# Optimization experiments

Measured on AMD Instinct MI355X. Metric: run time of the kernel, lower is better.

## Reference

```python
import jax, jax.numpy as jnp
import numpy as np

F = 26          # categorical fields
VOCAB = 10000   # per-field vocab
ED = 64         # embed_dim
NUM = 13        # numerical_num
B = 4096        # batch
E = 8           # expert_num
T = 2           # task_num
D = (F + 1) * ED            # embed_output_dim = 1728
BOT = [512, 256]
TOW = [128, 64]


def setup_inputs() -> dict:
    key = jax.random.key(0)
    ks = jax.random.split(key, 20)
    s = 0.02
    inp = {}
    inp['categorical_x'] = jax.random.randint(ks[0], (B, F), 0, VOCAB, dtype=jnp.int64 if jax.config.read('jax_enable_x64') else jnp.int32)
    inp['numerical_x'] = jax.random.normal(ks[1], (B, NUM), dtype=jnp.float32)
    # shared embedding table with per-field offsets (pytorch-fm EmbeddingLayer)
    inp['offsets'] = jnp.arange(F, dtype=jnp.int32) * VOCAB
    inp['W_emb'] = jax.random.normal(ks[2], (F * VOCAB, ED), dtype=jnp.float32) * s
    # numerical linear
    inp['Wn'] = jax.random.normal(ks[3], (NUM, ED), dtype=jnp.float32) * s
    inp['bn'] = jnp.zeros((ED,), dtype=jnp.float32)
    # experts (stacked): D -> 512 -> 256, ReLU after each (BN/dropout identity at eval)
    inp['We1'] = jax.random.normal(ks[4], (E, D, BOT[0]), dtype=jnp.float32) * s
    inp['be1'] = jnp.zeros((E, BOT[0]), dtype=jnp.float32)
    inp['We2'] = jax.random.normal(ks[5], (E, BOT[0], BOT[1]), dtype=jnp.float32) * s
    inp['be2'] = jnp.zeros((E, BOT[1]), dtype=jnp.float32)
    # gates: D -> E with softmax
    inp['Wg'] = jax.random.normal(ks[6], (T, D, E), dtype=jnp.float32) * s
    inp['bg'] = jnp.zeros((T, E), dtype=jnp.float32)
    # towers: 256 -> 128 -> 64 -> 1
    inp['Wt1'] = jax.random.normal(ks[7], (T, BOT[1], TOW[0]), dtype=jnp.float32) * s
    inp['bt1'] = jnp.zeros((T, TOW[0]), dtype=jnp.float32)
    inp['Wt2'] = jax.random.normal(ks[8], (T, TOW[0], TOW[1]), dtype=jnp.float32) * s
    inp['bt2'] = jnp.zeros((T, TOW[1]), dtype=jnp.float32)
    inp['Wt3'] = jax.random.normal(ks[9], (T, TOW[1], 1), dtype=jnp.float32) * s
    inp['bt3'] = jnp.zeros((T, 1), dtype=jnp.float32)
    return inp


def reference(categorical_x, numerical_x, offsets, W_emb, Wn, bn,
              We1, be1, We2, be2, Wg, bg,
              Wt1, bt1, Wt2, bt2, Wt3, bt3):
    b = categorical_x.shape[0]
    cat_emb = W_emb[categorical_x + offsets[None, :]]          # [B, F, ED]
    num_emb = numerical_x @ Wn + bn                            # [B, ED]
    emb = jnp.concatenate([cat_emb, num_emb[:, None, :]], axis=1).reshape(b, -1)  # [B, D]
    # all experts on the shared embedding (duplicate() gives identical copies per task)
    h = jax.nn.relu(jnp.einsum('bd,edh->ebh', emb, We1) + be1[:, None, :])        # [E, B, 512]
    fea = jax.nn.relu(jnp.einsum('ebh,eho->ebo', h, We2) + be2[:, None, :])       # [E, B, 256]
    # per-task softmax gating and weighted expert mixing
    gate = jax.nn.softmax(jnp.einsum('bd,tde->tbe', emb, Wg) + bg[:, None, :], axis=-1)  # [T, B, E]
    task_fea = jnp.einsum('tbe,ebo->tbo', gate, fea)                              # [T, B, 256]
    # towers
    h1 = jax.nn.relu(jnp.einsum('tbo,toh->tbh', task_fea, Wt1) + bt1[:, None, :])
    h2 = jax.nn.relu(jnp.einsum('tbh,thk->tbk', h1, Wt2) + bt2[:, None, :])
    logits = jnp.einsum('tbk,tko->tbo', h2, Wt3) + bt3[:, None, :]                # [T, B, 1]
    return jax.nn.sigmoid(logits[..., 0])                                         # [T, B]
```

## Files before the change

### kernel.cpp

```cpp
#include <hip/hip_runtime.h>
#include <hip/hip_bf16.h>

#define B_SZ 4096
#define F_CAT 26
#define NUM_N 13
#define ED 64
#define D_DIM 1728
#define E_EXP 8
#define T_TASK 2
#define BOT0 512
#define BOT1 256
#define TOW0 128
#define TOW1 64

typedef __bf16 bf16x8 __attribute__((ext_vector_type(8)));
typedef float f32x4 __attribute__((ext_vector_type(4)));
typedef float f32x16 __attribute__((ext_vector_type(16)));
typedef long lx2 __attribute__((ext_vector_type(2)));
typedef int i32x4 __attribute__((ext_vector_type(4)));
typedef int i32x8 __attribute__((ext_vector_type(8)));

#define SCL 0x7F7F7F7F

__device__ __forceinline__ void gload_lds16(const void* g, void* l) {
  __builtin_amdgcn_global_load_lds(
      (const __attribute__((address_space(1))) void*)g,
      (__attribute__((address_space(3))) void*)l, 16, 0, 0);
}

#define BAR() do { asm volatile("" ::: "memory"); __builtin_amdgcn_s_barrier(); asm volatile("" ::: "memory"); } while (0)
#define VM6() asm volatile("s_waitcnt vmcnt(6)" ::: "memory")
#define VM4() asm volatile("s_waitcnt vmcnt(4)" ::: "memory")

__device__ __forceinline__ int permk(int k6) {
  return (k6 & 7) + (((k6 >> 3) & 3) << 4) + (((k6 >> 5) & 1) << 3);
}

__device__ __forceinline__ size_t mxpos(int row, int kabs, int K) {
  int kt = kabs >> 6, kk = kabs & 63;
  int reg = row & ~63, ro = row & 63;
  int sub = ro >> 5, rr = ro & 31, r = rr & 15;
  int u = ((kk >> 5) << 1) | ((rr >> 4) & 1);
  int p = (kk >> 4) & 1;
  int g = (sub << 1) | p;
  return (size_t)(reg + g * 16 + r) * K + kt * 64 + u * 16 + (kk & 15);
}

__device__ __forceinline__ unsigned char f2e4m3(float x) {
  unsigned su = (__float_as_uint(x) >> 24) & 0x80u;
  float ax = fabsf(x);
  if (!(ax < 448.f)) return (unsigned char)(su | 0x7E);
  if (ax == 0.f) return (unsigned char)su;
  int e;
  float m = frexpf(ax, &e);
  int E = e - 1;
  if (E < -6) {
    int mi = (int)rintf(ldexpf(ax, 9));
    if (mi >= 8) return (unsigned char)(su | 0x08);
    return (unsigned char)(su | mi);
  }
  int mi = (int)rintf(ldexpf(m, 4));
  if (mi == 16) { mi = 8; E += 1; if (E > 8) return (unsigned char)(su | 0x7E); }
  return (unsigned char)(su | ((E + 7) << 3) | (mi - 8));
}

__device__ __forceinline__ void trans_tile_bf16(
    const float* __restrict__ inp, __hip_bfloat16* __restrict__ outp,
    int R, int C, int cx, int ry, float (*tile)[33])
{
  int c0 = cx * 32, r0 = ry * 32;
  int tx = threadIdx.x & 31, ty = threadIdx.x >> 5;
#pragma unroll
  for (int i = 0; i < 32; i += 8)
    tile[ty + i][tx] = inp[(size_t)(r0 + ty + i) * C + c0 + tx];
  __syncthreads();
#pragma unroll
  for (int i = 0; i < 32; i += 8)
    outp[(size_t)(c0 + ty + i) * R + r0 + tx] = __float2bfloat16(tile[tx][ty + i]);
}

__device__ __forceinline__ void trans_tile_fp8mx(
    const float* __restrict__ inp, unsigned char* __restrict__ outp,
    int R, int C, int cx, int ry, float (*tile)[33])
{
  int c0 = cx * 32, r0 = ry * 32;
  int tx = threadIdx.x & 31, ty = threadIdx.x >> 5;
#pragma unroll
  for (int i = 0; i < 32; i += 8)
    tile[ty + i][tx] = inp[(size_t)(r0 + ty + i) * C + c0 + tx];
  __syncthreads();
  int ki = r0 + tx;
#pragma unroll
  for (int i = 0; i < 32; i += 8)
    outp[mxpos(c0 + ty + i, ki, R)] = f2e4m3(tile[tx][ty + i] * 16.f);
}

__global__ __launch_bounds__(256) void prep_weights(
    const float* __restrict__ We1, const float* __restrict__ We2,
    const float* __restrict__ Wg,
    unsigned char* __restrict__ We1T8, __hip_bfloat16* __restrict__ We2T,
    unsigned char* __restrict__ WgT8)
{
  __shared__ float tile[32][33];
  int id = blockIdx.x;
  if (id < 6912) {
    int z = id / 864, r = id - z * 864;
    int cx = r & 15, ry = r >> 4;
    trans_tile_fp8mx(We1 + (size_t)z * D_DIM * BOT0, We1T8 + (size_t)z * D_DIM * BOT0,
                     D_DIM, BOT0, cx, ry, tile);
  } else if (id < 7936) {
    int r2 = id - 6912;
    int z = r2 >> 7, r = r2 & 127;
    int cx = r & 7, ry = r >> 3;
    trans_tile_bf16(We2 + (size_t)z * BOT0 * BOT1, We2T + (size_t)z * BOT0 * BOT1,
                    BOT0, BOT1, cx, ry, tile);
  } else {
    int i = (id - 7936) * 256 + threadIdx.x;
    int n = i / D_DIM, d = i - n * D_DIM;
    int t = n >> 3, e2 = n & 7;
    int pd = (d & ~63) + permk(d & 63);
    WgT8[(size_t)n * D_DIM + pd] =
        f2e4m3(Wg[((size_t)t * D_DIM + d) * E_EXP + e2] * 16.f);
  }
}

__global__ __launch_bounds__(256) void embed_convert(
    const int* __restrict__ cat, const float* __restrict__ numx,
    const int* __restrict__ offsets, const float* __restrict__ W_emb,
    const float* __restrict__ Wn, const float* __restrict__ bnum,
    unsigned char* __restrict__ emb8)
{
  int W = blockIdx.x * 256 + threadIdx.x;
  int prow = W / 108, ucol = W - prow * 108;
  int f = ucol >> 2, u = ucol & 3;
  int reg = prow & ~63, po = prow & 63;
  int g = po >> 4, r = po & 15;
  int sub = g >> 1, p = g & 1;
  int h = u >> 1, rbit = u & 1;
  int b = reg + sub * 32 + rbit * 16 + r;
  int kk = h * 32 + p * 16;
  float vals[16];
  if (f < F_CAT) {
    int row = cat[(size_t)b * F_CAT + f] + offsets[f];
    const float4* src = reinterpret_cast<const float4*>(&W_emb[(size_t)row * ED + kk]);
#pragma unroll
    for (int q = 0; q < 4; ++q) {
      float4 v = src[q];
      vals[q * 4 + 0] = v.x; vals[q * 4 + 1] = v.y;
      vals[q * 4 + 2] = v.z; vals[q * 4 + 3] = v.w;
    }
  } else {
#pragma unroll
    for (int j = 0; j < 16; ++j) vals[j] = bnum[kk + j];
    for (int n = 0; n < NUM_N; ++n) {
      float x = numx[(size_t)b * NUM_N + n];
      const float* wr = &Wn[n * ED + kk];
#pragma unroll
      for (int j = 0; j < 16; ++j) vals[j] = fmaf(x, wr[j], vals[j]);
    }
  }
  union { unsigned char c[16]; uint4 q; } o;
#pragma unroll
  for (int j = 0; j < 16; ++j) o.c[j] = f2e4m3(vals[j] * 16.f);
  *reinterpret_cast<uint4*>(&emb8[(size_t)prow * D_DIM + f * 64 + u * 16]) = o.q;
}

__global__ __launch_bounds__(256) void gate_mfma(
    const unsigned char* __restrict__ emb8, const unsigned char* __restrict__ WgT8,
    const float* __restrict__ bg, float* __restrict__ gate)
{
  int wid = threadIdx.x >> 6, lane = threadIdx.x & 63;
  int l15 = lane & 15, lh = lane >> 4;
  int r0 = (blockIdx.x * 4 + wid) * 16;
  f32x4 acc = {};
  int b = r0 + l15;
  int reg = b & ~63, ro = b & 63;
  int sub = ro >> 5, rr = ro & 31;
  int rbit = (rr >> 4) & 1, rq = rr & 15;
  int pgh = lh >> 1;
  int prow = reg + (((sub << 1) | pgh) << 4) + rq;
  const unsigned char* arow = emb8 + (size_t)prow * D_DIM + rbit * 16 + (lh & 1) * 8;
  const unsigned char* brow = WgT8 + (size_t)l15 * D_DIM + lh * 16;
#pragma unroll 3
  for (int k = 0; k < D_DIM; k += 64) {
    long a0 = *reinterpret_cast<const long*>(arow + k);
    long a1 = *reinterpret_cast<const long*>(arow + k + 32);
    lx2 bv = *reinterpret_cast<const lx2*>(brow + k);
    acc = __builtin_amdgcn_mfma_f32_16x16x32_fp8_fp8(a0, bv[0], acc, 0, 0, 0);
    acc = __builtin_amdgcn_mfma_f32_16x16x32_fp8_fp8(a1, bv[1], acc, 0, 0, 0);
  }
  int t = l15 >> 3, e = l15 & 7;
  float bv = bg[t * E_EXP + e];
#pragma unroll
  for (int r = 0; r < 4; ++r) {
    float lg = acc[r] * (1.f / 256.f) + bv;
    float m = lg;
    m = fmaxf(m, __shfl_xor(m, 1));
    m = fmaxf(m, __shfl_xor(m, 2));
    m = fmaxf(m, __shfl_xor(m, 4));
    float ex = expf(lg - m);
    float s = ex;
    s += __shfl_xor(s, 1);
    s += __shfl_xor(s, 2);
    s += __shfl_xor(s, 4);
    int row = r0 + lh * 4 + r;
    gate[((size_t)t * B_SZ + row) * E_EXP + e] = ex / s;
  }
}

__device__ __forceinline__ void mfma16(const bf16x8* a, const bf16x8* b, f32x4 (*accRows)[4]) {
#pragma unroll
  for (int i = 0; i < 4; ++i)
#pragma unroll
    for (int j = 0; j < 4; ++j)
      accRows[i][j] = __builtin_amdgcn_mfma_f32_16x16x32_bf16(a[i], b[j], accRows[i][j], 0, 0, 0);
}

__device__ __forceinline__ i32x8 ld32(const char* base, int off) {
  i32x4 a = *reinterpret_cast<const i32x4*>(base + off);
  i32x4 b = *reinterpret_cast<const i32x4*>(base + off + 1024);
  i32x8 r;
  r[0] = a[0]; r[1] = a[1]; r[2] = a[2]; r[3] = a[3];
  r[4] = b[0]; r[5] = b[1]; r[6] = b[2]; r[7] = b[3];
  return r;
}

__global__ __launch_bounds__(512, 2) void gemm_mx(
    const unsigned char* __restrict__ A8, size_t strideAe,
    const unsigned char* __restrict__ BT8,
    const float* __restrict__ bias,
    __hip_bfloat16* __restrict__ C,
    int M, int N, int K)
{
  extern __shared__ char smem[];
  int e = blockIdx.z;
  const unsigned char* Ap = A8 + strideAe * (size_t)e;
  const unsigned char* Bp = BT8 + (size_t)e * N * K;
  const float* bp = bias + (size_t)e * N;
  __hip_bfloat16* Cp = C + (size_t)e * M * N;
  int bm0 = blockIdx.x * 256, bn0 = blockIdx.y * 256;

  int tid = threadIdx.x;
  int wid = tid >> 6, lane = tid & 63;
  int l15 = lane & 15, lh = lane >> 4;
  int l31 = lane & 31, hl = lane >> 5;
  int wrow = (wid >> 2) * 128, wcol = (wid & 3) * 64;

  int slotc = (lh ^ (((l15 >> 3) & 1) << 1)) << 4;
  const char* rdA = smem + (wrow + l15) * 64 + slotc;
  const char* rdB = smem + 49152 + (wcol + l15) * 64 + slotc;
  char* stA = smem + (wid << 10);
  char* stB = smem + 49152 + (wid << 10);

  int srow = tid >> 2;
  int ssw = (tid & 3) ^ (((srow >> 3) & 1) << 1);
  const unsigned char* gA0 = Ap + (size_t)(bm0 + srow) * K + ssw * 16;
  const unsigned char* gA1 = Ap + (size_t)(bm0 + 128 + srow) * K + ssw * 16;
  const unsigned char* gB0 = Bp + (size_t)(bn0 + srow) * K + ssw * 16;
  const unsigned char* gB1 = Bp + (size_t)(bn0 + 128 + srow) * K + ssw * 16;

  auto STAGE = [&](int koff, int buf) {
    gload_lds16(gA0 + koff, stA + buf * 16384);
    gload_lds16(gA1 + koff, stA + buf * 16384 + 8192);
    gload_lds16(gB0 + koff, stB + buf * 16384);
    gload_lds16(gB1 + koff, stB + buf * 16384 + 8192);
  };

  f32x16 acc[4][2] = {};
  int NT = K >> 6;

  STAGE(0, 0);
  STAGE(64, 1);
  VM4();
  BAR();

  int bufc = 0, koff = 128;
  for (int T = 0; T < NT; ++T) {
    const char* As = rdA + bufc * 16384;
    const char* Bs = rdB + bufc * 16384;
    int sb = bufc >= 1 ? bufc - 1 : 2;
    i32x8 va0, va1, vb0, vb1;

    va0 = ld32(As, 0);
    va1 = ld32(As, 2048);
    vb0 = ld32(Bs, 0);
    vb1 = ld32(Bs, 2048);
    STAGE(koff, sb);
    BAR();
    __builtin_amdgcn_s_setprio(1);
    acc[0][0] = __builtin_amdgcn_mfma_scale_f32_32x32x64_f8f6f4(va0, vb0, acc[0][0], 0, 0, 0, SCL, 0, SCL);
    acc[0][1] = __builtin_amdgcn_mfma_scale_f32_32x32x64_f8f6f4(va0, vb1, acc[0][1], 0, 0, 0, SCL, 0, SCL);
    acc[1][0] = __builtin_amdgcn_mfma_scale_f32_32x32x64_f8f6f4(va1, vb0, acc[1][0], 0, 0, 0, SCL, 0, SCL);
    acc[1][1] = __builtin_amdgcn_mfma_scale_f32_32x32x64_f8f6f4(va1, vb1, acc[1][1], 0, 0, 0, SCL, 0, SCL);
    __builtin_amdgcn_s_setprio(0);
    BAR();

    va0 = ld32(As, 4096);
    va1 = ld32(As, 4096 + 2048);
    BAR();
    __builtin_amdgcn_s_setprio(1);
    acc[2][0] = __builtin_amdgcn_mfma_scale_f32_32x32x64_f8f6f4(va0, vb0, acc[2][0], 0, 0, 0, SCL, 0, SCL);
    acc[2][1] = __builtin_amdgcn_mfma_scale_f32_32x32x64_f8f6f4(va0, vb1, acc[2][1], 0, 0, 0, SCL, 0, SCL);
    acc[3][0] = __builtin_amdgcn_mfma_scale_f32_32x32x64_f8f6f4(va1, vb0, acc[3][0], 0, 0, 0, SCL, 0, SCL);
    acc[3][1] = __builtin_amdgcn_mfma_scale_f32_32x32x64_f8f6f4(va1, vb1, acc[3][1], 0, 0, 0, SCL, 0, SCL);
    __builtin_amdgcn_s_setprio(0);
    VM4();
    BAR();

    koff += 64;
    bufc = bufc == 2 ? 0 : bufc + 1;
  }

  asm volatile("s_waitcnt vmcnt(0)" ::: "memory");
  BAR();
  __hip_bfloat16* cs = (__hip_bfloat16*)smem;
#pragma unroll
  for (int mi = 0; mi < 4; ++mi) {
#pragma unroll
    for (int nj = 0; nj < 2; ++nj) {
      int colT = wcol + nj * 32 + l31;
      float bv = bp[bn0 + colT];
      f32x16 a = acc[mi][nj];
#pragma unroll
      for (int rg = 0; rg < 16; ++rg) {
        int rowT = wrow + mi * 32 + (rg & 3) + ((rg >> 2) << 3) + (hl << 2);
        float v = a[rg] * (1.f / 256.f) + bv;
        cs[(size_t)rowT * 256 + colT] = __float2bfloat16(fmaxf(v, 0.f));
      }
    }
  }
  BAR();
  {
    int rr = tid >> 5, c8 = (tid & 31) * 8;
#pragma unroll
    for (int p = 0; p < 16; ++p) {
      int row = p * 16 + rr;
      *reinterpret_cast<uint4*>(&Cp[(size_t)(bm0 + row) * N + bn0 + c8]) =
          *reinterpret_cast<const uint4*>(&cs[(size_t)row * 256 + c8]);
    }
  }
}

__global__ __launch_bounds__(512, 2) void gemm4p(
    const __hip_bfloat16* __restrict__ A, size_t strideAe,
    const __hip_bfloat16* __restrict__ BT,
    const float* __restrict__ bias,
    __hip_bfloat16* __restrict__ C,
    int M, int N, int K)
{
  extern __shared__ char smem[];
  int e = blockIdx.z;
  const __hip_bfloat16* Ap = A + strideAe * (size_t)e;
  const __hip_bfloat16* Bp = BT + (size_t)e * N * K;
  const float* bp = bias + (size_t)e * N;
  __hip_bfloat16* Cp = C + (size_t)e * M * N;
  int bm0 = blockIdx.x * 128, bn0 = blockIdx.y * 256;

  int tid = threadIdx.x;
  int wid = tid >> 6, lane = tid & 63;
  int l15 = lane & 15, lh = lane >> 4;
  int wrow = (wid >> 2) * 64, wcol = (wid & 3) * 64;

  int slotc = (lh ^ (((l15 >> 3) & 1) << 1)) << 4;
  const char* rdA = smem + (wrow + l15) * 64 + slotc;
  const char* rdB = smem + 32768 + (wcol + l15) * 64 + slotc;
  char* stA = smem + (wid << 10);
  char* stB = smem + 32768 + (wid << 10);

  const __hip_bfloat16* gA;
  const __hip_bfloat16* gB[2];
  {
    int X = (wid << 10) + (lane << 4);
    int row = X >> 6;
    int ss = ((X >> 4) & 3) ^ (((row >> 3) & 1) << 1);
    gA = Ap + (size_t)(bm0 + row) * K + ss * 8;
#pragma unroll
    for (int j = 0; j < 2; ++j) {
      int X2 = X + (j << 13);
      int row2 = X2 >> 6;
      int ss2 = ((X2 >> 4) & 3) ^ (((row2 >> 3) & 1) << 1);
      gB[j] = Bp + (size_t)(bn0 + row2) * K + ss2 * 8;
    }
  }

  f32x4 acc[4][4] = {};
  int NT = K >> 6;

  gload_lds16(gA, stA);
#pragma unroll
  for (int j = 0; j < 2; ++j) gload_lds16(gB[j], stB + (j << 13));
  gload_lds16(gA + 32, stA + 8192);
#pragma unroll
  for (int j = 0; j < 2; ++j) gload_lds16(gB[j] + 32, stB + 16384 + (j << 13));
  gload_lds16(gA + 64, stA + 16384);
#pragma unroll
  for (int j = 0; j < 2; ++j) gload_lds16(gB[j] + 64, stB + 32768 + (j << 13));
  VM6();
  BAR();

  for (int T = 0; T < NT; ++T) {
    int pA = (T & 1) << 14, qA = pA ^ 16384;
    int pB = (T & 1) << 15, qB = pB ^ 32768;
    const char* As = rdA + pA;
    const char* Bs = rdB + pB;
    bf16x8 a[4], b[4];

#pragma unroll
    for (int i = 0; i < 4; ++i) a[i] = *(const bf16x8*)(As + i * 1024);
#pragma unroll
    for (int j = 0; j < 4; ++j) b[j] = *(const bf16x8*)(Bs + j * 1024);
    gload_lds16(gA + 96, stA + qA + 8192);
#pragma unroll
    for (int j = 0; j < 2; ++j) gload_lds16(gB[j] + 96, stB + qB + 16384 + (j << 13));
    BAR();
    __builtin_amdgcn_s_setprio(1); mfma16(a, b, acc); __builtin_amdgcn_s_setprio(0);
    VM6();
    BAR();

#pragma unroll
    for (int i = 0; i < 4; ++i) a[i] = *(const bf16x8*)(As + 8192 + i * 1024);
#pragma unroll
    for (int j = 0; j < 4; ++j) b[j] = *(const bf16x8*)(Bs + 16384 + j * 1024);
    gload_lds16(gA + 128, stA + pA);
#pragma unroll
    for (int j = 0; j < 2; ++j) gload_lds16(gB[j] + 128, stB + pB + (j << 13));
    BAR();
    __builtin_amdgcn_s_setprio(1); mfma16(a, b, acc); __builtin_amdgcn_s_setprio(0);
    VM6();
    BAR();

    gA += 64;
#pragma unroll
    for (int j = 0; j < 2; ++j) gB[j] += 64;
  }

  asm volatile("s_waitcnt vmcnt(0)" ::: "memory");
  BAR();
  __hip_bfloat16* cs = (__hip_bfloat16*)smem;
#pragma unroll
  for (int nj = 0; nj < 4; ++nj) {
    int col = wcol + nj * 16 + l15;
    float bv = bp[bn0 + col];
#pragma unroll
    for (int mi = 0; mi < 4; ++mi) {
      int rb = wrow + mi * 16 + lh * 4;
#pragma unroll
      for (int r = 0; r < 4; ++r) {
        float v = acc[mi][nj][r] + bv;
        cs[(size_t)(rb + r) * 256 + col] = __float2bfloat16(fmaxf(v, 0.f));
      }
    }
  }
  BAR();
  {
    int rr = tid >> 5, c8 = (tid & 31) * 8;
#pragma unroll
    for (int p = 0; p < 8; ++p) {
      int row = p * 16 + rr;
      *reinterpret_cast<uint4*>(&Cp[(size_t)(bm0 + row) * N + bn0 + c8]) =
          *reinterpret_cast<const uint4*>(&cs[(size_t)row * 256 + c8]);
    }
  }
}

#define TB 16
__global__ __launch_bounds__(256) void combine_tower(
    const float* __restrict__ gate, const __hip_bfloat16* __restrict__ fea,
    const float* __restrict__ Wt1, const float* __restrict__ bt1,
    const float* __restrict__ Wt2, const float* __restrict__ bt2,
    const float* __restrict__ Wt3, const float* __restrict__ bt3,
    float* __restrict__ out)
{
  int t = blockIdx.y;
  int b0 = blockIdx.x * TB;
  int tid = threadIdx.x;
  __shared__ float gs[TB][E_EXP];
  __shared__ float tf[TB][BOT1];
  __shared__ float h1[TB][TOW0];
  __shared__ float h2[TB][TOW1];
  if (tid < TB * E_EXP) {
    int bl = tid >> 3, e = tid & 7;
    gs[bl][e] = gate[((size_t)t * B_SZ + b0 + bl) * E_EXP + e];
  }
  __syncthreads();
  for (int i = tid; i < TB * BOT1; i += 256) {
    int bl = i >> 8, o = i & 255;
    float s = 0.f;
#pragma unroll
    for (int e = 0; e < E_EXP; ++e)
      s = fmaf(gs[bl][e], __bfloat162float(fea[((size_t)e * B_SZ + b0 + bl) * BOT1 + o]), s);
    tf[bl][o] = s;
  }
  __syncthreads();
  {
    int h = tid & 127, half = tid >> 7;
    float a[8] = {0, 0, 0, 0, 0, 0, 0, 0};
    for (int d = 0; d < BOT1; ++d) {
      float w = Wt1[((size_t)t * BOT1 + d) * TOW0 + h];
#pragma unroll
      for (int q = 0; q < 8; ++q) a[q] = fmaf(w, tf[half * 8 + q][d], a[q]);
    }
    float bv = bt1[t * TOW0 + h];
#pragma unroll
    for (int q = 0; q < 8; ++q) h1[half * 8 + q][h] = fmaxf(a[q] + bv, 0.f);
  }
  __syncthreads();
  {
    int h = tid & 63, qt = tid >> 6;
    float a[4] = {0, 0, 0, 0};
    for (int d = 0; d < TOW0; ++d) {
      float w = Wt2[((size_t)t * TOW0 + d) * TOW1 + h];
#pragma unroll
      for (int q = 0; q < 4; ++q) a[q] = fmaf(w, h1[qt * 4 + q][d], a[q]);
    }
    float bv = bt2[t * TOW1 + h];
#pragma unroll
    for (int q = 0; q < 4; ++q) h2[qt * 4 + q][h] = fmaxf(a[q] + bv, 0.f);
  }
  __syncthreads();
  {
    int l16 = tid & 15, bl = tid >> 4;
    float p = 0.f;
#pragma unroll
    for (int d = l16; d < TOW1; d += 16) p = fmaf(h2[bl][d], Wt3[t * TOW1 + d], p);
#pragma unroll
    for (int o = 8; o; o >>= 1) p += __shfl_down(p, o, 16);
    if (l16 == 0) {
      float lg = p + bt3[t];
      out[(size_t)t * B_SZ + b0 + bl] = 1.f / (1.f + expf(-lg));
    }
  }
}

extern "C" void kernel_launch(void* const* d_in, const int* in_sizes, int n_in,
                              void* d_out, int out_size, void* d_ws, size_t ws_size,
                              hipStream_t stream) {
  const int* cat = (const int*)d_in[0];
  const float* numx = (const float*)d_in[1];
  const int* offsets = (const int*)d_in[2];
  const float* W_emb = (const float*)d_in[3];
  const float* Wn = (const float*)d_in[4];
  const float* bnv = (const float*)d_in[5];
  const float* We1 = (const float*)d_in[6];
  const float* be1 = (const float*)d_in[7];
  const float* We2 = (const float*)d_in[8];
  const float* be2 = (const float*)d_in[9];
  const float* Wg = (const float*)d_in[10];
  const float* bg = (const float*)d_in[11];
  const float* Wt1 = (const float*)d_in[12];
  const float* bt1 = (const float*)d_in[13];
  const float* Wt2 = (const float*)d_in[14];
  const float* bt2 = (const float*)d_in[15];
  const float* Wt3 = (const float*)d_in[16];
  const float* bt3 = (const float*)d_in[17];
  float* out = (float*)d_out;

  char* ws = (char*)d_ws;
  size_t off = 0;
  auto alloc = [&](size_t bytes) {
    char* p = ws + off;
    off += (bytes + 255) & ~(size_t)255;
    return p;
  };
  unsigned char*  emb8  = (unsigned char*)alloc((size_t)B_SZ * D_DIM);
  unsigned char*  We1T8 = (unsigned char*)alloc((size_t)E_EXP * BOT0 * D_DIM);
  __hip_bfloat16* We2T  = (__hip_bfloat16*)alloc((size_t)E_EXP * BOT1 * BOT0 * 2);
  __hip_bfloat16* H     = (__hip_bfloat16*)alloc((size_t)E_EXP * B_SZ * BOT0 * 2);
  __hip_bfloat16* fea   = (__hip_bfloat16*)alloc((size_t)E_EXP * B_SZ * BOT1 * 2);
  float* gate = (float*)alloc((size_t)T_TASK * B_SZ * E_EXP * 4);
  unsigned char*  WgT8  = (unsigned char*)alloc((size_t)T_TASK * E_EXP * D_DIM);
  (void)alloc(4096);

  hipFuncSetAttribute((const void*)gemm_mx,
                      hipFuncAttributeMaxDynamicSharedMemorySize, 131072);
  hipFuncSetAttribute((const void*)gemm4p,
                      hipFuncAttributeMaxDynamicSharedMemorySize, 98304);

  prep_weights<<<dim3(8044), 256, 0, stream>>>(We1, We2, Wg, We1T8, We2T, WgT8);

  embed_convert<<<dim3(B_SZ * 108 / 256), 256, 0, stream>>>(
      cat, numx, offsets, W_emb, Wn, bnv, emb8);

  gate_mfma<<<dim3(B_SZ / 64), 256, 0, stream>>>(emb8, WgT8, bg, gate);

  gemm_mx<<<dim3(B_SZ / 256, BOT0 / 256, E_EXP), 512, 131072, stream>>>(
      emb8, (size_t)0, We1T8, be1, H, B_SZ, BOT0, D_DIM);

  gemm4p<<<dim3(B_SZ / 128, BOT1 / 256, E_EXP), 512, 98304, stream>>>(
      H, (size_t)B_SZ * BOT0, We2T, be2, fea, B_SZ, BOT1, BOT0);

  combine_tower<<<dim3(B_SZ / TB, T_TASK), 256, 0, stream>>>(
      gate, fea, Wt1, bt1, Wt2, bt2, Wt3, bt3, out);
}
```

Before: 117.7 us.

## Quantize expert hidden layer and second GEMM to MX fp8

The first expert GEMM now writes its ReLU output as fp8 e4m3, pre-swizzled into the MX layout the next GEMM reads. The second expert GEMM moves from a bf16 16x16x32 MFMA kernel to a new 128-row fp8 scaled-MFMA kernel, and the We2 weights are prepared as fp8. This halves the traffic for the large H intermediate and the second GEMM's operands, and uses the higher-rate fp8 matrix instructions. In exchange, the hidden activations are quantized more coarsely, and the first GEMM's epilogue does a per-element scattered fp8 conversion.

```diff
diff --git a/kernel.cpp b/kernel.cpp
--- a/kernel.cpp
+++ b/kernel.cpp
@@ -29,8 +29,8 @@
 }
 
 #define BAR() do { asm volatile("" ::: "memory"); __builtin_amdgcn_s_barrier(); asm volatile("" ::: "memory"); } while (0)
-#define VM6() asm volatile("s_waitcnt vmcnt(6)" ::: "memory")
 #define VM4() asm volatile("s_waitcnt vmcnt(4)" ::: "memory")
+#define VM3() asm volatile("s_waitcnt vmcnt(3)" ::: "memory")
 
 __device__ __forceinline__ int permk(int k6) {
   return (k6 & 7) + (((k6 >> 3) & 3) << 4) + (((k6 >> 5) & 1) << 3);
@@ -64,21 +64,6 @@
   return (unsigned char)(su | ((E + 7) << 3) | (mi - 8));
 }
 
-__device__ __forceinline__ void trans_tile_bf16(
-    const float* __restrict__ inp, __hip_bfloat16* __restrict__ outp,
-    int R, int C, int cx, int ry, float (*tile)[33])
-{
-  int c0 = cx * 32, r0 = ry * 32;
-  int tx = threadIdx.x & 31, ty = threadIdx.x >> 5;
-#pragma unroll
-  for (int i = 0; i < 32; i += 8)
-    tile[ty + i][tx] = inp[(size_t)(r0 + ty + i) * C + c0 + tx];
-  __syncthreads();
-#pragma unroll
-  for (int i = 0; i < 32; i += 8)
-    outp[(size_t)(c0 + ty + i) * R + r0 + tx] = __float2bfloat16(tile[tx][ty + i]);
-}
-
 __device__ __forceinline__ void trans_tile_fp8mx(
     const float* __restrict__ inp, unsigned char* __restrict__ outp,
     int R, int C, int cx, int ry, float (*tile)[33])
@@ -98,7 +83,7 @@
 __global__ __launch_bounds__(256) void prep_weights(
     const float* __restrict__ We1, const float* __restrict__ We2,
     const float* __restrict__ Wg,
-    unsigned char* __restrict__ We1T8, __hip_bfloat16* __restrict__ We2T,
+    unsigned char* __restrict__ We1T8, unsigned char* __restrict__ We2T8,
     unsigned char* __restrict__ WgT8)
 {
   __shared__ float tile[32][33];
@@ -112,8 +97,8 @@
     int r2 = id - 6912;
     int z = r2 >> 7, r = r2 & 127;
     int cx = r & 7, ry = r >> 3;
-    trans_tile_bf16(We2 + (size_t)z * BOT0 * BOT1, We2T + (size_t)z * BOT0 * BOT1,
-                    BOT0, BOT1, cx, ry, tile);
+    trans_tile_fp8mx(We2 + (size_t)z * BOT0 * BOT1, We2T8 + (size_t)z * BOT0 * BOT1,
+                     BOT0, BOT1, cx, ry, tile);
   } else {
     int i = (id - 7936) * 256 + threadIdx.x;
     int n = i / D_DIM, d = i - n * D_DIM;
@@ -208,14 +193,6 @@
   }
 }
 
-__device__ __forceinline__ void mfma16(const bf16x8* a, const bf16x8* b, f32x4 (*accRows)[4]) {
-#pragma unroll
-  for (int i = 0; i < 4; ++i)
-#pragma unroll
-    for (int j = 0; j < 4; ++j)
-      accRows[i][j] = __builtin_amdgcn_mfma_f32_16x16x32_bf16(a[i], b[j], accRows[i][j], 0, 0, 0);
-}
-
 __device__ __forceinline__ i32x8 ld32(const char* base, int off) {
   i32x4 a = *reinterpret_cast<const i32x4*>(base + off);
   i32x4 b = *reinterpret_cast<const i32x4*>(base + off + 1024);
@@ -225,7 +202,135 @@
   return r;
 }
 
+#define MXMFMA(va, vb, c) \
+  __builtin_amdgcn_mfma_scale_f32_32x32x64_f8f6f4(va, vb, c, 0, 0, 0, SCL, 0, SCL)
+
 __global__ __launch_bounds__(512, 2) void gemm_mx(
+    const unsigned char* __restrict__ A8, size_t strideAe,
+    const unsigned char* __restrict__ BT8,
+    const float* __restrict__ bias,
+    unsigned char* __restrict__ C8,
+    int M, int N, int K)
+{
+  extern __shared__ char smem[];
+  int e = blockIdx.z;
+  const unsigned char* Ap = A8 + strideAe * (size_t)e;
+  const unsigned char* Bp = BT8 + (size_t)e * N * K;
+  const float* bp = bias + (size_t)e * N;
+  unsigned char* Cp8 = C8 + (size_t)e * M * N;
+  int bm0 = blockIdx.x * 256, bn0 = blockIdx.y * 256;
+
+  int tid = threadIdx.x;
+  int wid = tid >> 6, lane = tid & 63;
+  int l15 = lane & 15, lh = lane >> 4;
+  int l31 = lane & 31, hl = lane >> 5;
+  int wrow = (wid >> 2) * 128, wcol = (wid & 3) * 64;
+
+  int slotc = (lh ^ (((l15 >> 3) & 1) << 1)) << 4;
+  const char* rdA = smem + (wrow + l15) * 64 + slotc;
+  const char* rdB = smem + 49152 + (wcol + l15) * 64 + slotc;
+  char* stA = smem + (wid << 10);
+  char* stB = smem + 49152 + (wid << 10);
+
+  int srow = tid >> 2;
+  int ssw = (tid & 3) ^ (((srow >> 3) & 1) << 1);
+  const unsigned char* gA0 = Ap + (size_t)(bm0 + srow) * K + ssw * 16;
+  const unsigned char* gA1 = Ap + (size_t)(bm0 + 128 + srow) * K + ssw * 16;
+  const unsigned char* gB0 = Bp + (size_t)(bn0 + srow) * K + ssw * 16;
+  const unsigned char* gB1 = Bp + (size_t)(bn0 + 128 + srow) * K + ssw * 16;
+
+  auto STAGE = [&](int koff, int buf) {
+    gload_lds16(gA0 + koff, stA + buf * 16384);
+    gload_lds16(gA1 + koff, stA + buf * 16384 + 8192);
+    gload_lds16(gB0 + koff, stB + buf * 16384);
+    gload_lds16(gB1 + koff, stB + buf * 16384 + 8192);
+  };
+
+  f32x16 acc[4][2] = {};
+  int NT = K >> 6;
+
+  STAGE(0, 0);
+  STAGE(64, 1);
+  VM4();
+  BAR();
+
+  int bufc = 0, koff = 128;
+  for (int T = 0; T < NT; ++T) {
+    const char* As = rdA + bufc * 16384;
+    const char* Bs = rdB + bufc * 16384;
+    int sb = bufc >= 1 ? bufc - 1 : 2;
+    i32x8 va0, va1, vb0, vb1;
+
+    va0 = ld32(As, 0);
+    va1 = ld32(As, 2048);
+    vb0 = ld32(Bs, 0);
+    vb1 = ld32(Bs, 2048);
+    STAGE(koff, sb);
+    BAR();
+    __builtin_amdgcn_s_setprio(1);
+    acc[0][0] = MXMFMA(va0, vb0, acc[0][0]);
+    acc[0][1] = MXMFMA(va0, vb1, acc[0][1]);
+    acc[1][0] = MXMFMA(va1, vb0, acc[1][0]);
+    acc[1][1] = MXMFMA(va1, vb1, acc[1][1]);
+    __builtin_amdgcn_s_setprio(0);
+    BAR();
+
+    va0 = ld32(As, 4096);
+    va1 = ld32(As, 4096 + 2048);
+    BAR();
+    __builtin_amdgcn_s_setprio(1);
+    acc[2][0] = MXMFMA(va0, vb0, acc[2][0]);
+    acc[2][1] = MXMFMA(va0, vb1, acc[2][1]);
+    acc[3][0] = MXMFMA(va1, vb0, acc[3][0]);
+    acc[3][1] = MXMFMA(va1, vb1, acc[3][1]);
+    __builtin_amdgcn_s_setprio(0);
+    VM4();
+    BAR();
+
+    koff += 64;
+    bufc = bufc == 2 ? 0 : bufc + 1;
+  }
+
+  asm volatile("s_waitcnt vmcnt(0)" ::: "memory");
+  BAR();
+  unsigned char* cs8 = (unsigned char*)smem;
+#pragma unroll
+  for (int mi = 0; mi < 4; ++mi) {
+#pragma unroll
+    for (int nj = 0; nj < 2; ++nj) {
+      int colT = wcol + nj * 32 + l31;
+      float bv = bp[bn0 + colT];
+      int kk = colT & 63;
+      int ktrel = colT >> 6;
+      int p = (kk >> 4) & 1;
+      int ubase = (kk >> 5) << 1;
+      int b4 = kk & 15;
+      f32x16 a = acc[mi][nj];
+#pragma unroll
+      for (int rg = 0; rg < 16; ++rg) {
+        int rowT = wrow + mi * 32 + (rg & 3) + ((rg >> 2) << 3) + (hl << 2);
+        float v = fmaxf(a[rg] * (1.f / 256.f) + bv, 0.f);
+        int regrel = rowT & ~63, ro = rowT & 63;
+        int sub = ro >> 5, rr2 = ro & 31, r = rr2 & 15;
+        int u = ubase | ((rr2 >> 4) & 1);
+        int g = (sub << 1) | p;
+        cs8[(regrel + g * 16 + r) * 256 + ktrel * 64 + u * 16 + b4] = f2e4m3(v * 16.f);
+      }
+    }
+  }
+  BAR();
+  {
+    int rr = tid >> 4, c16 = (tid & 15) * 16;
+#pragma unroll
+    for (int p2 = 0; p2 < 8; ++p2) {
+      int row = p2 * 32 + rr;
+      *reinterpret_cast<uint4*>(&Cp8[(size_t)(bm0 + row) * N + bn0 + c16]) =
+          *reinterpret_cast<const uint4*>(&cs8[(size_t)row * 256 + c16]);
+    }
+  }
+}
+
+__global__ __launch_bounds__(512, 2) void gemm_mx128(
     const unsigned char* __restrict__ A8, size_t strideAe,
     const unsigned char* __restrict__ BT8,
     const float* __restrict__ bias,
@@ -238,73 +343,65 @@
   const unsigned char* Bp = BT8 + (size_t)e * N * K;
   const float* bp = bias + (size_t)e * N;
   __hip_bfloat16* Cp = C + (size_t)e * M * N;
-  int bm0 = blockIdx.x * 256, bn0 = blockIdx.y * 256;
+  int bm0 = blockIdx.x * 128;
 
   int tid = threadIdx.x;
   int wid = tid >> 6, lane = tid & 63;
   int l15 = lane & 15, lh = lane >> 4;
   int l31 = lane & 31, hl = lane >> 5;
-  int wrow = (wid >> 2) * 128, wcol = (wid & 3) * 64;
+  int wrow = (wid >> 2) * 64, wcol = (wid & 3) * 64;
 
   int slotc = (lh ^ (((l15 >> 3) & 1) << 1)) << 4;
   const char* rdA = smem + (wrow + l15) * 64 + slotc;
-  const char* rdB = smem + 49152 + (wcol + l15) * 64 + slotc;
+  const char* rdB = smem + 24576 + (wcol + l15) * 64 + slotc;
   char* stA = smem + (wid << 10);
-  char* stB = smem + 49152 + (wid << 10);
+  char* stB = smem + 24576 + (wid << 10);
 
   int srow = tid >> 2;
   int ssw = (tid & 3) ^ (((srow >> 3) & 1) << 1);
   const unsigned char* gA0 = Ap + (size_t)(bm0 + srow) * K + ssw * 16;
-  const unsigned char* gA1 = Ap + (size_t)(bm0 + 128 + srow) * K + ssw * 16;
-  const unsigned char* gB0 = Bp + (size_t)(bn0 + srow) * K + ssw * 16;
-  const unsigned char* gB1 = Bp + (size_t)(bn0 + 128 + srow) * K + ssw * 16;
+  const unsigned char* gB0 = Bp + (size_t)srow * K + ssw * 16;
+  const unsigned char* gB1 = Bp + (size_t)(128 + srow) * K + ssw * 16;
 
   auto STAGE = [&](int koff, int buf) {
-    gload_lds16(gA0 + koff, stA + buf * 16384);
-    gload_lds16(gA1 + koff, stA + buf * 16384 + 8192);
+    gload_lds16(gA0 + koff, stA + buf * 8192);
     gload_lds16(gB0 + koff, stB + buf * 16384);
     gload_lds16(gB1 + koff, stB + buf * 16384 + 8192);
   };
 
-  f32x16 acc[4][2] = {};
+  f32x16 acc[2][2] = {};
   int NT = K >> 6;
 
   STAGE(0, 0);
   STAGE(64, 1);
-  VM4();
+  VM3();
   BAR();
 
   int bufc = 0, koff = 128;
   for (int T = 0; T < NT; ++T) {
-    const char* As = rdA + bufc * 16384;
+    const char* As = rdA + bufc * 8192;
     const char* Bs = rdB + bufc * 16384;
     int sb = bufc >= 1 ? bufc - 1 : 2;
-    i32x8 va0, va1, vb0, vb1;
-
-    va0 = ld32(As, 0);
-    va1 = ld32(As, 2048);
+    i32x8 va, vb0, vb1;
+
+    va = ld32(As, 0);
     vb0 = ld32(Bs, 0);
     vb1 = ld32(Bs, 2048);
     STAGE(koff, sb);
     BAR();
     __builtin_amdgcn_s_setprio(1);
-    acc[0][0] = __builtin_amdgcn_mfma_scale_f32_32x32x64_f8f6f4(va0, vb0, acc[0][0], 0, 0, 0, SCL, 0, SCL);
-    acc[0][1] = __builtin_amdgcn_mfma_scale_f32_32x32x64_f8f6f4(va0, vb1, acc[0][1], 0, 0, 0, SCL, 0, SCL);
-    acc[1][0] = __builtin_amdgcn_mfma_scale_f32_32x32x64_f8f6f4(va1, vb0, acc[1][0], 0, 0, 0, SCL, 0, SCL);
-    acc[1][1] = __builtin_amdgcn_mfma_scale_f32_32x32x64_f8f6f4(va1, vb1, acc[1][1], 0, 0, 0, SCL, 0, SCL);
+    acc[0][0] = MXMFMA(va, vb0, acc[0][0]);
+    acc[0][1] = MXMFMA(va, vb1, acc[0][1]);
     __builtin_amdgcn_s_setprio(0);
     BAR();
 
-    va0 = ld32(As, 4096);
-    va1 = ld32(As, 4096 + 2048);
+    va = ld32(As, 2048);
     BAR();
     __builtin_amdgcn_s_setprio(1);
-    acc[2][0] = __builtin_amdgcn_mfma_scale_f32_32x32x64_f8f6f4(va0, vb0, acc[2][0], 0, 0, 0, SCL, 0, SCL);
-    acc[2][1] = __builtin_amdgcn_mfma_scale_f32_32x32x64_f8f6f4(va0, vb1, acc[2][1], 0, 0, 0, SCL, 0, SCL);
-    acc[3][0] = __builtin_amdgcn_mfma_scale_f32_32x32x64_f8f6f4(va1, vb0, acc[3][0], 0, 0, 0, SCL, 0, SCL);
-    acc[3][1] = __builtin_amdgcn_mfma_scale_f32_32x32x64_f8f6f4(va1, vb1, acc[3][1], 0, 0, 0, SCL, 0, SCL);
+    acc[1][0] = MXMFMA(va, vb0, acc[1][0]);
+    acc[1][1] = MXMFMA(va, vb1, acc[1][1]);
     __builtin_amdgcn_s_setprio(0);
-    VM4();
+    VM3();
     BAR();
 
     koff += 64;
@@ -315,11 +412,11 @@
   BAR();
   __hip_bfloat16* cs = (__hip_bfloat16*)smem;
 #pragma unroll
-  for (int mi = 0; mi < 4; ++mi) {
+  for (int mi = 0; mi < 2; ++mi) {
 #pragma unroll
     for (int nj = 0; nj < 2; ++nj) {
       int colT = wcol + nj * 32 + l31;
-      float bv = bp[bn0 + colT];
+      float bv = bp[colT];
       f32x16 a = acc[mi][nj];
 #pragma unroll
       for (int rg = 0; rg < 16; ++rg) {
@@ -333,131 +430,9 @@
   {
     int rr = tid >> 5, c8 = (tid & 31) * 8;
 #pragma unroll
-    for (int p = 0; p < 16; ++p) {
-      int row = p * 16 + rr;
-      *reinterpret_cast<uint4*>(&Cp[(size_t)(bm0 + row) * N + bn0 + c8]) =
-          *reinterpret_cast<const uint4*>(&cs[(size_t)row * 256 + c8]);
-    }
-  }
-}
-
-__global__ __launch_bounds__(512, 2) void gemm4p(
-    const __hip_bfloat16* __restrict__ A, size_t strideAe,
-    const __hip_bfloat16* __restrict__ BT,
-    const float* __restrict__ bias,
-    __hip_bfloat16* __restrict__ C,
-    int M, int N, int K)
-{
-  extern __shared__ char smem[];
-  int e = blockIdx.z;
-  const __hip_bfloat16* Ap = A + strideAe * (size_t)e;
-  const __hip_bfloat16* Bp = BT + (size_t)e * N * K;
-  const float* bp = bias + (size_t)e * N;
-  __hip_bfloat16* Cp = C + (size_t)e * M * N;
-  int bm0 = blockIdx.x * 128, bn0 = blockIdx.y * 256;
-
-  int tid = threadIdx.x;
-  int wid = tid >> 6, lane = tid & 63;
-  int l15 = lane & 15, lh = lane >> 4;
-  int wrow = (wid >> 2) * 64, wcol = (wid & 3) * 64;
-
-  int slotc = (lh ^ (((l15 >> 3) & 1) << 1)) << 4;
-  const char* rdA = smem + (wrow + l15) * 64 + slotc;
-  const char* rdB = smem + 32768 + (wcol + l15) * 64 + slotc;
-  char* stA = smem + (wid << 10);
-  char* stB = smem + 32768 + (wid << 10);
-
-  const __hip_bfloat16* gA;
-  const __hip_bfloat16* gB[2];
-  {
-    int X = (wid << 10) + (lane << 4);
-    int row = X >> 6;
-    int ss = ((X >> 4) & 3) ^ (((row >> 3) & 1) << 1);
-    gA = Ap + (size_t)(bm0 + row) * K + ss * 8;
-#pragma unroll
-    for (int j = 0; j < 2; ++j) {
-      int X2 = X + (j << 13);
-      int row2 = X2 >> 6;
-      int ss2 = ((X2 >> 4) & 3) ^ (((row2 >> 3) & 1) << 1);
-      gB[j] = Bp + (size_t)(bn0 + row2) * K + ss2 * 8;
-    }
-  }
-
-  f32x4 acc[4][4] = {};
-  int NT = K >> 6;
-
-  gload_lds16(gA, stA);
-#pragma unroll
-  for (int j = 0; j < 2; ++j) gload_lds16(gB[j], stB + (j << 13));
-  gload_lds16(gA + 32, stA + 8192);
-#pragma unroll
-  for (int j = 0; j < 2; ++j) gload_lds16(gB[j] + 32, stB + 16384 + (j << 13));
-  gload_lds16(gA + 64, stA + 16384);
-#pragma unroll
-  for (int j = 0; j < 2; ++j) gload_lds16(gB[j] + 64, stB + 32768 + (j << 13));
-  VM6();
-  BAR();
-
-  for (int T = 0; T < NT; ++T) {
-    int pA = (T & 1) << 14, qA = pA ^ 16384;
-    int pB = (T & 1) << 15, qB = pB ^ 32768;
-    const char* As = rdA + pA;
-    const char* Bs = rdB + pB;
-    bf16x8 a[4], b[4];
-
-#pragma unroll
-    for (int i = 0; i < 4; ++i) a[i] = *(const bf16x8*)(As + i * 1024);
-#pragma unroll
-    for (int j = 0; j < 4; ++j) b[j] = *(const bf16x8*)(Bs + j * 1024);
-    gload_lds16(gA + 96, stA + qA + 8192);
-#pragma unroll
-    for (int j = 0; j < 2; ++j) gload_lds16(gB[j] + 96, stB + qB + 16384 + (j << 13));
-    BAR();
-    __builtin_amdgcn_s_setprio(1); mfma16(a, b, acc); __builtin_amdgcn_s_setprio(0);
-    VM6();
-    BAR();
-
-#pragma unroll
-    for (int i = 0; i < 4; ++i) a[i] = *(const bf16x8*)(As + 8192 + i * 1024);
-#pragma unroll
-    for (int j = 0; j < 4; ++j) b[j] = *(const bf16x8*)(Bs + 16384 + j * 1024);
-    gload_lds16(gA + 128, stA + pA);
-#pragma unroll
-    for (int j = 0; j < 2; ++j) gload_lds16(gB[j] + 128, stB + pB + (j << 13));
-    BAR();
-    __builtin_amdgcn_s_setprio(1); mfma16(a, b, acc); __builtin_amdgcn_s_setprio(0);
-    VM6();
-    BAR();
-
-    gA += 64;
-#pragma unroll
-    for (int j = 0; j < 2; ++j) gB[j] += 64;
-  }
-
-  asm volatile("s_waitcnt vmcnt(0)" ::: "memory");
-  BAR();
-  __hip_bfloat16* cs = (__hip_bfloat16*)smem;
-#pragma unroll
-  for (int nj = 0; nj < 4; ++nj) {
-    int col = wcol + nj * 16 + l15;
-    float bv = bp[bn0 + col];
-#pragma unroll
-    for (int mi = 0; mi < 4; ++mi) {
-      int rb = wrow + mi * 16 + lh * 4;
-#pragma unroll
-      for (int r = 0; r < 4; ++r) {
-        float v = acc[mi][nj][r] + bv;
-        cs[(size_t)(rb + r) * 256 + col] = __float2bfloat16(fmaxf(v, 0.f));
-      }
-    }
-  }
-  BAR();
-  {
-    int rr = tid >> 5, c8 = (tid & 31) * 8;
-#pragma unroll
-    for (int p = 0; p < 8; ++p) {
-      int row = p * 16 + rr;
-      *reinterpret_cast<uint4*>(&Cp[(size_t)(bm0 + row) * N + bn0 + c8]) =
+    for (int p2 = 0; p2 < 8; ++p2) {
+      int row = p2 * 16 + rr;
+      *reinterpret_cast<uint4*>(&Cp[(size_t)(bm0 + row) * N + c8]) =
           *reinterpret_cast<const uint4*>(&cs[(size_t)row * 256 + c8]);
     }
   }
@@ -564,30 +539,30 @@
   };
   unsigned char*  emb8  = (unsigned char*)alloc((size_t)B_SZ * D_DIM);
   unsigned char*  We1T8 = (unsigned char*)alloc((size_t)E_EXP * BOT0 * D_DIM);
-  __hip_bfloat16* We2T  = (__hip_bfloat16*)alloc((size_t)E_EXP * BOT1 * BOT0 * 2);
-  __hip_bfloat16* H     = (__hip_bfloat16*)alloc((size_t)E_EXP * B_SZ * BOT0 * 2);
+  unsigned char*  We2T8 = (unsigned char*)alloc((size_t)E_EXP * BOT1 * BOT0);
+  unsigned char*  H8    = (unsigned char*)alloc((size_t)E_EXP * B_SZ * BOT0);
   __hip_bfloat16* fea   = (__hip_bfloat16*)alloc((size_t)E_EXP * B_SZ * BOT1 * 2);
   float* gate = (float*)alloc((size_t)T_TASK * B_SZ * E_EXP * 4);
   unsigned char*  WgT8  = (unsigned char*)alloc((size_t)T_TASK * E_EXP * D_DIM);
   (void)alloc(4096);
 
   hipFuncSetAttribute((const void*)gemm_mx,
-                      hipFuncAttributeMaxDynamicSharedMemorySize, 131072);
-  hipFuncSetAttribute((const void*)gemm4p,
                       hipFuncAttributeMaxDynamicSharedMemorySize, 98304);
-
-  prep_weights<<<dim3(8044), 256, 0, stream>>>(We1, We2, Wg, We1T8, We2T, WgT8);
+  hipFuncSetAttribute((const void*)gemm_mx128,
+                      hipFuncAttributeMaxDynamicSharedMemorySize, 73728);
+
+  prep_weights<<<dim3(8044), 256, 0, stream>>>(We1, We2, Wg, We1T8, We2T8, WgT8);
 
   embed_convert<<<dim3(B_SZ * 108 / 256), 256, 0, stream>>>(
       cat, numx, offsets, W_emb, Wn, bnv, emb8);
 
   gate_mfma<<<dim3(B_SZ / 64), 256, 0, stream>>>(emb8, WgT8, bg, gate);
 
-  gemm_mx<<<dim3(B_SZ / 256, BOT0 / 256, E_EXP), 512, 131072, stream>>>(
-      emb8, (size_t)0, We1T8, be1, H, B_SZ, BOT0, D_DIM);
-
-  gemm4p<<<dim3(B_SZ / 128, BOT1 / 256, E_EXP), 512, 98304, stream>>>(
-      H, (size_t)B_SZ * BOT0, We2T, be2, fea, B_SZ, BOT1, BOT0);
+  gemm_mx<<<dim3(B_SZ / 256, BOT0 / 256, E_EXP), 512, 98304, stream>>>(
+      emb8, (size_t)0, We1T8, be1, H8, B_SZ, BOT0, D_DIM);
+
+  gemm_mx128<<<dim3(B_SZ / 128, 1, E_EXP), 512, 73728, stream>>>(
+      H8, (size_t)B_SZ * BOT0, We2T8, be2, fea, B_SZ, BOT1, BOT0);
 
   combine_tower<<<dim3(B_SZ / TB, T_TASK), 256, 0, stream>>>(
       gate, fea, Wt1, bt1, Wt2, bt2, Wt3, bt3, out);
```

Measured after the change: 135.9 us. +15.5%, slower.
